# Optimization experiments

Hardware: AMD Instinct MI355X
Metric: run time of the kernel (lower is better)

The kernel has to match this reference:

```python
import jax, jax.numpy as jnp
import numpy as np

L = 8192            # sequence length
V = 100000          # vocab size
E = 256             # embedding dim
H = 512             # lstm hidden dim (bidirectional total)
HD = H // 2         # per-direction hidden
TAGS = 32
T = TAGS + 2        # tagset + START/STOP
START = T - 2       # START_TAG = -2
STOP = T - 1        # STOP_TAG = -1
NEG = -10000.0


def setup_inputs() -> dict:
    key = jax.random.key(0)
    ks = jax.random.split(key, 11)
    s = 0.05
    return {
        "input_words": jax.random.randint(ks[0], (L,), 0, V),
        "embed": jax.random.normal(ks[1], (V, E), dtype=jnp.float32) * s,
        "Wih_f": jax.random.normal(ks[2], (4 * HD, E), dtype=jnp.float32) * s,
        "Whh_f": jax.random.normal(ks[3], (4 * HD, HD), dtype=jnp.float32) * s,
        "b_f": jax.random.normal(ks[4], (4 * HD,), dtype=jnp.float32) * s,
        "Wih_b": jax.random.normal(ks[5], (4 * HD, E), dtype=jnp.float32) * s,
        "Whh_b": jax.random.normal(ks[6], (4 * HD, HD), dtype=jnp.float32) * s,
        "b_b": jax.random.normal(ks[7], (4 * HD,), dtype=jnp.float32) * s,
        "W_out": jax.random.normal(ks[8], (T, H), dtype=jnp.float32) * s,
        "b_out": jax.random.normal(ks[9], (T,), dtype=jnp.float32) * s,
        "transitions": jax.random.normal(ks[10], (T, T), dtype=jnp.float32),
    }


def _lstm_dir(x, Wih, Whh, b, reverse):
    # single-layer LSTM, one direction; torch gate order i, f, g, o
    def step(carry, xt):
        h, c = carry
        g = xt @ Wih.T + h @ Whh.T + b
        i, f, gg, o = jnp.split(g, 4)
        i = jax.nn.sigmoid(i)
        f = jax.nn.sigmoid(f)
        gg = jnp.tanh(gg)
        o = jax.nn.sigmoid(o)
        c = f * c + i * gg
        h = o * jnp.tanh(c)
        return (h, c), h

    init = (jnp.zeros((HD,), x.dtype), jnp.zeros((HD,), x.dtype))
    _, hs = jax.lax.scan(step, init, x, reverse=reverse)
    return hs  # (L, HD)


def _crf_marginals(feats, transitions):
    lse = jax.nn.logsumexp
    # forward algorithm: alpha_t[j] = lse_i(alpha_{t-1}[i] + trans[j,i]) + feat_t[j]
    def fstep(alpha, feat):
        new = lse(alpha[None, :] + transitions, axis=1) + feat
        return new, new

    alpha0 = jnp.full((T,), NEG, feats.dtype).at[START].set(0.0)
    alphaL, log_alpha = jax.lax.scan(fstep, alpha0, feats)  # (L, T)

    # backward algorithm, replicating repo's init: beta_L[j] = lse_i(trans[i, j])
    beta_last = lse(transitions, axis=0)

    # beta_t[j] = lse_i(beta_{t+1}[i] + feat_{t+1}[i] + trans[i, j])
    def bstep(beta, feat_next):
        new = lse((beta + feat_next)[:, None] + transitions, axis=0)
        return new, new

    _, betas = jax.lax.scan(bstep, beta_last, feats[1:], reverse=True)
    log_beta = jnp.concatenate([betas, beta_last[None]], axis=0)  # (L, T)
    return log_alpha + log_beta


def reference(input_words, embed, Wih_f, Whh_f, b_f, Wih_b, Whh_b, b_b,
              W_out, b_out, transitions):
    x = embed[input_words]                           # (L, E)
    hf = _lstm_dir(x, Wih_f, Whh_f, b_f, reverse=False)
    hb = _lstm_dir(x, Wih_b, Whh_b, b_b, reverse=True)
    lstm_out = jnp.concatenate([hf, hb], axis=-1)    # (L, H)
    feats = lstm_out @ W_out.T + b_out               # (L, T)
    score = _crf_marginals(feats, transitions)       # (L, T)
    tags = jnp.argmax(score, axis=1)                 # (L,)
    return score, tags
```

## Files before the change

kernel.cpp:

```cpp
#include <hip/hip_runtime.h>
#include <cstdint>
#include <cstddef>

#define LSEQ 8192
#define NT   34
#define NP   36
#define SCH  64
#define CCH  128
#define F_L2E 1.4426950408889634f
#define F_LN2 0.6931471805599453f

typedef int v4i __attribute__((ext_vector_type(4)));

#if __has_builtin(__builtin_amdgcn_global_load_lds)
#define HAS_GLL 1
#else
#define HAS_GLL 0
#endif

__device__ __forceinline__ float ex2(float x){
#if __has_builtin(__builtin_amdgcn_exp2f)
  return __builtin_amdgcn_exp2f(x);
#else
  return exp2f(x);
#endif
}
__device__ __forceinline__ float lg2(float x){
#if __has_builtin(__builtin_amdgcn_logf)
  return __builtin_amdgcn_logf(x);
#else
  return __log2f(x);
#endif
}

__device__ __forceinline__ float sigf(float x){
  return __fdividef(1.f, 1.f + ex2(-F_L2E * x));
}
__device__ __forceinline__ float tanhf_fast(float x){
  return 1.f - __fdividef(2.f, ex2(2.f * F_L2E * x) + 1.f);
}

__device__ __forceinline__ v4i mfma_i8(v4i a, v4i b, v4i c){
  asm("v_mfma_i32_16x16x64_i8 %0, %1, %2, %0" : "+v"(c) : "v"(a), "v"(b));
  return c;
}

__device__ __forceinline__ void barrier_lds(){
  asm volatile("s_waitcnt lgkmcnt(0)\n\ts_barrier" ::: "memory");
}

__global__ void k_quant(const float* __restrict__ Whh_f,
                        const float* __restrict__ Whh_b,
                        int* __restrict__ Wq, float* __restrict__ fac){
  int bid = blockIdx.x;
  int dir = bid >> 10;
  int r   = bid & 1023;
  int i   = threadIdx.x;
  const float* W = (dir ? Whh_b : Whh_f) + r * 256 + i * 4;
  float w0 = W[0], w1 = W[1], w2 = W[2], w3 = W[3];
  float m = fmaxf(fmaxf(fabsf(w0), fabsf(w1)), fmaxf(fabsf(w2), fabsf(w3)));
  for (int s = 32; s; s >>= 1) m = fmaxf(m, __shfl_xor(m, s));
  float scale = (m > 0.f) ? m / 127.f : 1.f;
  float inv = __fdividef(1.f, scale);
  int q0 = (int)rintf(w0 * inv), q1 = (int)rintf(w1 * inv);
  int q2 = (int)rintf(w2 * inv), q3 = (int)rintf(w3 * inv);
  q0 = max(-127, min(127, q0)); q1 = max(-127, min(127, q1));
  q2 = max(-127, min(127, q2)); q3 = max(-127, min(127, q3));
  int p = (q0 & 255) | ((q1 & 255) << 8) | ((q2 & 255) << 16) | ((q3 & 255) << 24);
  Wq[(dir << 16) + (r << 6) + i] = p;
  if (i == 0) fac[(dir << 10) + r] = scale * (1.f / 127.f);
}

__global__ void k_gproj(const int* __restrict__ words,
                        const float* __restrict__ embed,
                        const float* __restrict__ Wih_f, const float* __restrict__ b_f,
                        const float* __restrict__ Wih_b, const float* __restrict__ b_b,
                        float* __restrict__ G_f, float* __restrict__ G_b){
  int dir = blockIdx.y;
  const float* Wih = dir ? Wih_b : Wih_f;
  const float* bb  = dir ? b_b  : b_f;
  float* G = dir ? G_b : G_f;
  int t0 = blockIdx.x * 16;
  __shared__ __align__(16) float X[16 * 256];
  for (int idx = threadIdx.x; idx < 16 * 256; idx += 256) {
    int tt = idx >> 8, e = idx & 255;
    X[idx] = embed[(size_t)words[t0 + tt] * 256 + e];
  }
  __syncthreads();
  const float4* X4 = (const float4*)X;
  for (int rb = 0; rb < 4; rb++) {
    int r = rb * 256 + threadIdx.x;
    float bv = bb[r];
    float acc[16];
#pragma unroll
    for (int tt = 0; tt < 16; tt++) acc[tt] = bv;
    const float4* W4 = (const float4*)(Wih + (size_t)r * 256);
    for (int eb = 0; eb < 64; eb++) {
      float4 w = W4[eb];
#pragma unroll
      for (int tt = 0; tt < 16; tt++) {
        float4 x = X4[tt * 64 + eb];
        acc[tt] += w.x * x.x + w.y * x.y + w.z * x.z + w.w * x.w;
      }
    }
    for (int tt = 0; tt < 16; tt++)
      G[(size_t)(t0 + tt) * 1024 + (threadIdx.x << 2) + rb] = acc[tt];
  }
}

__global__ __launch_bounds__(512, 2) void k_lstm(const int* __restrict__ Wq,
                                                 const float* __restrict__ fac,
                                                 const float* __restrict__ G_f,
                                                 const float* __restrict__ G_b,
                                                 float* __restrict__ hf,
                                                 float* __restrict__ hb){
  int dir = blockIdx.x;
  const int* Wqd = Wq + (dir << 16);
  const float* facp = fac + (dir << 10);
  const float* G = dir ? G_b : G_f;
  float* hout = dir ? hb : hf;
  int tid = threadIdx.x;
  int ln  = tid & 63;
  int wv  = tid >> 6;
  int lg  = ln >> 4;
  int lr  = ln & 15;

  __shared__ __align__(16) float GL[2][4 * 1024];
  __shared__ __align__(16) int h8c[2][64];
  __shared__ __align__(16) int graw[1024];

  v4i wgt[4][2][4];
#pragma unroll
  for (int g = 0; g < 4; g++)
#pragma unroll
    for (int h = 0; h < 2; h++) {
      int R = g * 256 + wv * 32 + h * 16 + lr;
#pragma unroll
      for (int ks = 0; ks < 4; ks++)
        wgt[g][h][ks] = *(const v4i*)(Wqd + R * 64 + ks * 16 + lg * 4);
    }

  float fI = 0.f, fF = 0.f, fG = 0.f, fO = 0.f;
  if (tid < 256) {
    fI = facp[tid]; fF = facp[tid + 256];
    fG = facp[tid + 512]; fO = facp[tid + 768];
  }
  if (tid < 64) h8c[0][tid] = 0;
  float c = 0.f;
  v4i zero = {0, 0, 0, 0};

  auto stage = [&](int cn) {
    int half = cn & 1;
    int gt0 = dir ? (8191 - (cn * 4 + 3)) : (cn * 4);
    const char* src = (const char*)(G + (size_t)gt0 * 1024) + (wv << 11) + (ln << 4);
    char* dst = (char*)&GL[half][0] + (wv << 11);
#pragma unroll
    for (int i = 0; i < 2; i++) {
#if HAS_GLL
      __builtin_amdgcn_global_load_lds(
          (const __attribute__((address_space(1))) unsigned int*)(src + (i << 10)),
          (__attribute__((address_space(3))) unsigned int*)(dst + (i << 10)),
          16, 0, 0);
#else
      *(float4*)(dst + (i << 10) + (ln << 4)) = *(const float4*)(src + (i << 10));
#endif
    }
  };

  auto stepA = [&](const int* hbuf) {
    const v4i* hb4 = (const v4i*)hbuf;
    v4i b0 = hb4[lg], b1 = hb4[4 + lg], b2 = hb4[8 + lg], b3 = hb4[12 + lg];
#pragma unroll
    for (int g = 0; g < 4; g++)
#pragma unroll
      for (int h = 0; h < 2; h++) {
        v4i a = mfma_i8(wgt[g][h][0], b0, zero);
        a = mfma_i8(wgt[g][h][1], b1, a);
        a = mfma_i8(wgt[g][h][2], b2, a);
        a = mfma_i8(wgt[g][h][3], b3, a);
        if (lr == 0)
          *(v4i*)&graw[g * 256 + wv * 32 + h * 16 + lg * 4] = a;
      }
  };

  stage(0);
  asm volatile("s_waitcnt vmcnt(0)" ::: "memory");
  __syncthreads();

  int cur = 0;
  for (int cn = 0; cn < 2048; ++cn) {
    if (cn + 1 < 2048) stage(cn + 1);
    const float* Hc = GL[cn & 1];
#pragma unroll
    for (int s = 0; s < 4; ++s) {
      int row = dir ? (3 - s) : s;
      int t = (cn << 2) + s;
      stepA(h8c[cur]);
      barrier_lds();
      if (tid < 256) {
        int u = tid;
        int aI = graw[u], aF = graw[256 + u], aG = graw[512 + u], aO = graw[768 + u];
        float4 gv = ((const float4*)(Hc + (row << 10)))[u];
        float ri = (float)aI * fI + gv.x;
        float rf = (float)aF * fF + gv.y;
        float rg = (float)aG * fG + gv.z;
        float ro = (float)aO * fO + gv.w;
        float is = sigf(ri), fs = sigf(rf);
        float gt = tanhf_fast(rg), os = sigf(ro);
        c = fs * c + is * gt;
        float hv = os * tanhf_fast(c);
        int time = dir ? (8191 - t) : t;
        hout[(size_t)time * 256 + u] = hv;
        ((signed char*)h8c[cur ^ 1])[u] = (signed char)(int)rintf(hv * 127.f);
      }
      cur ^= 1;
      if (s == 3) {
        asm volatile("s_waitcnt vmcnt(0) lgkmcnt(0)\n\ts_barrier" ::: "memory");
      } else {
        barrier_lds();
      }
    }
  }
}

__global__ void k_feats(const float* __restrict__ hf, const float* __restrict__ hb,
                        const float* __restrict__ W_out, const float* __restrict__ b_out,
                        float* __restrict__ feats){
  int t0 = blockIdx.x * 16;
  for (int oi = threadIdx.x; oi < 16 * NT; oi += 256) {
    int tt = oi / NT;
    int tag = oi - tt * NT;
    int t = t0 + tt;
    const float4* w4 = (const float4*)(W_out + (size_t)tag * 512);
    const float4* a4 = (const float4*)(hf + (size_t)t * 256);
    const float4* c4 = (const float4*)(hb + (size_t)t * 256);
    float acc = b_out[tag];
    for (int k = 0; k < 64; k++) {
      float4 w = w4[k]; float4 h = a4[k];
      acc += w.x * h.x + w.y * h.y + w.z * h.z + w.w * h.w;
    }
    for (int k = 0; k < 64; k++) {
      float4 w = w4[64 + k]; float4 h = c4[k];
      acc += w.x * h.x + w.y * h.y + w.z * h.z + w.w * h.w;
    }
    feats[(size_t)t * NT + tag] = acc;
  }
}

__global__ __launch_bounds__(320) void k_crf_p1(const float* __restrict__ feats,
                                                const float* __restrict__ trans,
                                                float* __restrict__ Pg,
                                                float* __restrict__ rmaxG){
  int dir = blockIdx.x >> 7;
  int c   = blockIdx.x & (CCH - 1);
  int tid = threadIdx.x;
  int t0  = c * SCH;

  __shared__ __align__(16) float TRM[NT * NP];
  __shared__ float Fe[(SCH + 1) * NT];
  __shared__ __align__(16) float Pbuf[2][NT * NP];
  __shared__ float CM[NP];
  __shared__ float RMs[NT];

  for (int idx = tid; idx < NT * NT; idx += 320) {
    int j = idx / NT, k = idx - j * NT;
    float v = (dir == 0) ? trans[j * NT + k] : trans[k * NT + j];
    TRM[j * NP + k] = v * F_L2E;
  }
  for (int idx = tid; idx < (SCH + 1) * NT; idx += 320) {
    int s = idx / NT, j = idx - s * NT;
    int t = t0 + s; if (t > LSEQ - 1) t = LSEQ - 1;
    Fe[idx] = feats[(size_t)t * NT + j] * F_L2E;
  }
  for (int idx = tid; idx < NT * NP; idx += 320) {
    int k = idx / NP, i = idx - k * NP;
    Pbuf[0][idx] = (i < NT && i == k) ? 0.f : -1e30f;
  }
  if (tid < NP) CM[tid] = (tid < NT) ? 0.f : -1e30f;
  __syncthreads();
  if (tid < NT) {
    float m = -3e38f;
    for (int k = 0; k < NT; k++) m = fmaxf(m, TRM[tid * NP + k]);
    RMs[tid] = m;
  }
  __syncthreads();
  for (int idx = tid; idx < NT * NT; idx += 320) {
    int j = idx / NT, k = idx - j * NT;
    TRM[j * NP + k] -= RMs[j];
  }
  __syncthreads();

  int cur = 0;
  int j = tid / 9, g = tid - (tid / 9) * 9;
  bool act = (tid < 306);
  int i0 = 4 * g;

  for (int s = 0; s < SCH; s++) {
    int t = (dir == 0) ? (t0 + s) : (t0 + SCH - 1 - s);
    if (dir == 1 && t == LSEQ - 1) continue;
    const float* Pc = Pbuf[cur];
    float* Pn = Pbuf[cur ^ 1];
    if (act) {
      float cm0 = CM[i0], cm1 = CM[i0 + 1], cm2 = CM[i0 + 2], cm3 = CM[i0 + 3];
      float s0 = 0, s1 = 0, s2 = 0, s3 = 0;
      const float* trp = TRM + j * NP;
      const float* fep = Fe + (t + 1 - t0) * NT;
#pragma unroll
      for (int k = 0; k < NT; k++) {
        float trv = trp[k];
        if (dir == 1) trv += fep[k];
        float4 p = *(const float4*)&Pc[k * NP + i0];
        s0 += ex2(trv + p.x - cm0);
        s1 += ex2(trv + p.y - cm1);
        s2 += ex2(trv + p.z - cm2);
        s3 += ex2(trv + p.w - cm3);
      }
      float base = RMs[j] + ((dir == 0) ? Fe[(t - t0) * NT + j] : 0.f);
      float4 o;
      o.x = base + cm0 + lg2(s0);
      o.y = base + cm1 + lg2(s1);
      o.z = (i0 + 2 < NT) ? (base + cm2 + lg2(s2)) : -1e30f;
      o.w = (i0 + 3 < NT) ? (base + cm3 + lg2(s3)) : -1e30f;
      *(float4*)&Pn[j * NP + i0] = o;
    }
    __syncthreads();
    if (tid < NP) {
      float m = -3e38f;
      const float* col = Pn + tid;
      for (int k = 0; k < NT; k++) m = fmaxf(m, col[k * NP]);
      CM[tid] = m;
    }
    cur ^= 1;
    __syncthreads();
  }

  const float* Pf = Pbuf[cur];
  size_t base = (size_t)((dir << 7) + c) * (NT * NP);
  for (int idx = tid; idx < NT * NP; idx += 320)
    Pg[base + idx] = Pf[idx];
  if (tid < NT) {
    float m = -3e38f;
    for (int i = 0; i < NT; i++) m = fmaxf(m, Pf[tid * NP + i]);
    rmaxG[((dir << 7) + c) * NT + tid] = m;
  }
}

__global__ void k_crf_p2(const float* __restrict__ trans,
                         const float* __restrict__ Pg,
                         const float* __restrict__ rmaxG,
                         float* __restrict__ vIn){
  int dir = blockIdx.x;
  int lane = threadIdx.x;
  bool a = (lane < NT);
  int j = a ? lane : 0;
  __shared__ float V[NP];

  float v;
  if (dir == 0) {
    v = (lane == 32) ? 0.f : -10000.f * F_L2E;
  } else {
    float m = -3e38f;
    for (int i = 0; i < NT; i++) m = fmaxf(m, trans[i * NT + j]);
    float s = 0.f;
    for (int i = 0; i < NT; i++) s += ex2((trans[i * NT + j] - m) * F_L2E);
    v = m * F_L2E + lg2(s);
  }
  if (lane < NP) V[lane] = -1e30f;
  barrier_lds();
  if (a) V[j] = v;
  barrier_lds();
  float vm = a ? v : -3e38f;
  for (int off = 32; off; off >>= 1) vm = fmaxf(vm, __shfl_xor(vm, off));

  if (a) {
    int c0 = (dir == 0) ? 0 : (CCH - 1);
    vIn[((size_t)(dir << 7) + c0) * NP + j] = v;
  }

  for (int it = 0; it < CCH - 1; it++) {
    int c = (dir == 0) ? it : (CCH - 1 - it);
    const float* row = Pg + ((size_t)(dir << 7) + c) * (NT * NP) + j * NP;
    float rm = rmaxG[((dir << 7) + c) * NT + j];
    float m = rm + vm;
    float s = 0.f;
#pragma unroll
    for (int k = 0; k < NP; k += 4) {
      float4 p = *(const float4*)&row[k];
      s += ex2(p.x + V[k]     - m);
      s += ex2(p.y + V[k + 1] - m);
      s += ex2(p.z + V[k + 2] - m);
      s += ex2(p.w + V[k + 3] - m);
    }
    float nv = m + lg2(s);
    if (a) V[j] = nv;
    barrier_lds();
    float x = a ? nv : -3e38f;
    for (int off = 32; off; off >>= 1) x = fmaxf(x, __shfl_xor(x, off));
    vm = x;
    int cn = (dir == 0) ? (c + 1) : (c - 1);
    if (a) vIn[((size_t)(dir << 7) + cn) * NP + j] = nv;
  }
}

__global__ void k_crf_p3(const float* __restrict__ feats,
                         const float* __restrict__ trans,
                         const float* __restrict__ vIn,
                         float* __restrict__ wsA,
                         float* __restrict__ wsB){
  int dir = blockIdx.x >> 7;
  int c   = blockIdx.x & (CCH - 1);
  int lane = threadIdx.x;
  int t0 = c * SCH;
  bool a = (lane < NT);
  int j = a ? lane : 0;
  __shared__ float A[NP];
  __shared__ float U[NP];

  float trr[NT];
  float rm = -3e38f;
#pragma unroll
  for (int k = 0; k < NT; k++) {
    float vv = (dir == 0) ? trans[j * NT + k] : trans[k * NT + j];
    trr[k] = vv * F_L2E;
    rm = fmaxf(rm, trr[k]);
  }
  if (lane < NP) { A[lane] = -1e30f; U[lane] = -1e30f; }
  float v0 = vIn[((size_t)(dir << 7) + c) * NP + j];
  barrier_lds();
  if (a) A[j] = v0;
  barrier_lds();
  float am = a ? v0 : -3e38f;
  for (int off = 32; off; off >>= 1) am = fmaxf(am, __shfl_xor(am, off));

  if (dir == 0) {
    float fe = feats[(size_t)t0 * NT + j] * F_L2E;
    for (int s = 0; s < SCH; s++) {
      int t = t0 + s;
      int tn = (t + 1 < LSEQ) ? t + 1 : LSEQ - 1;
      float fe_n = feats[(size_t)tn * NT + j] * F_L2E;
      float m = rm + am;
      float ss = 0.f;
#pragma unroll
      for (int k = 0; k < NT; k++) ss += ex2(trr[k] + A[k] - m);
      float out = m + lg2(ss) + fe;
      if (a) wsA[(size_t)t * NT + j] = out * F_LN2;
      if (a) A[j] = out;
      barrier_lds();
      float x = a ? out : -3e38f;
      for (int off = 32; off; off >>= 1) x = fmaxf(x, __shfl_xor(x, off));
      am = x;
      fe = fe_n;
    }
  } else {
    float b = v0;
    int tfirst = t0 + SCH; if (tfirst > LSEQ - 1) tfirst = LSEQ - 1;
    float fe = feats[(size_t)tfirst * NT + j] * F_L2E;
    for (int s = 0; s < SCH; s++) {
      int t = t0 + SCH - 1 - s;
      float fe_n = feats[(size_t)t * NT + j] * F_L2E;
      float out;
      if (t == LSEQ - 1) {
        out = b;
      } else {
        if (a) U[j] = b + fe;
        barrier_lds();
        float um = a ? U[j] : -3e38f;
        for (int off = 32; off; off >>= 1) um = fmaxf(um, __shfl_xor(um, off));
        float m = rm + um;
        float ss = 0.f;
#pragma unroll
        for (int k = 0; k < NT; k++) ss += ex2(trr[k] + U[k] - m);
        out = m + lg2(ss);
        barrier_lds();
      }
      if (a) wsB[(size_t)t * NT + j] = out * F_LN2;
      b = out;
      fe = fe_n;
    }
  }
}

__global__ void k_finish(const float* __restrict__ wsA, const float* __restrict__ wsB,
                         float* __restrict__ out){
  int t = blockIdx.x * 256 + threadIdx.x;
  float m = -3e38f; int bi = 0;
  for (int i = 0; i < NT; i++) {
    float sc = wsA[(size_t)t * NT + i] + wsB[(size_t)t * NT + i];
    out[(size_t)t * NT + i] = sc;
    if (sc > m) { m = sc; bi = i; }
  }
  out[(size_t)LSEQ * NT + t] = (float)bi;
}

extern "C" void kernel_launch(void* const* d_in, const int* in_sizes, int n_in,
                              void* d_out, int out_size, void* d_ws, size_t ws_size,
                              hipStream_t stream) {
  const int*   words  = (const int*)  d_in[0];
  const float* embed  = (const float*)d_in[1];
  const float* Wih_f  = (const float*)d_in[2];
  const float* Whh_f  = (const float*)d_in[3];
  const float* b_f    = (const float*)d_in[4];
  const float* Wih_b  = (const float*)d_in[5];
  const float* Whh_b  = (const float*)d_in[6];
  const float* b_b    = (const float*)d_in[7];
  const float* W_out  = (const float*)d_in[8];
  const float* b_out  = (const float*)d_in[9];
  const float* trans  = (const float*)d_in[10];
  float* out = (float*)d_out;

  float* wsf = (float*)d_ws;
  size_t off = 0;
  float* G_f   = wsf + off; off += (size_t)LSEQ * 1024;
  float* G_b   = wsf + off; off += (size_t)LSEQ * 1024;
  float* hf    = wsf + off; off += (size_t)LSEQ * 256;
  float* hb    = wsf + off; off += (size_t)LSEQ * 256;
  float* feats = wsf + off; off += (size_t)LSEQ * NT + 16;
  float* wsA   = wsf + off; off += (size_t)LSEQ * NT + 16;
  float* wsB   = wsf + off; off += (size_t)LSEQ * NT + 16;
  float* fac   = wsf + off; off += 2048;
  int*   Wq    = (int*)(wsf + off); off += 2 * 1024 * 64;
  float* Pg    = G_f;
  float* rmaxG = G_f + 256 * (NT * NP);
  float* vIn   = rmaxG + 256 * NT + 32;

  k_quant<<<2048, 64, 0, stream>>>(Whh_f, Whh_b, Wq, fac);
  k_gproj<<<dim3(512, 2), 256, 0, stream>>>(words, embed, Wih_f, b_f, Wih_b, b_b, G_f, G_b);
  k_lstm<<<2, 512, 0, stream>>>(Wq, fac, G_f, G_b, hf, hb);
  k_feats<<<512, 256, 0, stream>>>(hf, hb, W_out, b_out, feats);
  k_crf_p1<<<256, 320, 0, stream>>>(feats, trans, Pg, rmaxG);
  k_crf_p2<<<2, 64, 0, stream>>>(trans, Pg, rmaxG, vIn);
  k_crf_p3<<<256, 64, 0, stream>>>(feats, trans, vIn, wsA, wsB);
  k_finish<<<32, 256, 0, stream>>>(wsA, wsB, out);
}
```

Measured before the change: 8.705 ms.

## Apply LSTM gate nonlinearities in MFMA registers, removing LDS gate round-trip and barrier

Each lane now takes its gate pre-activations straight from the MFMA result registers by selecting the right row and component, instead of writing them to a shared graw buffer, synchronising, and reading them back. All 512 threads compute the cell update redundantly (two lanes per unit) and pack the int8 hidden state with DPP lane adds before one lane writes it. This removes one LDS barrier and the graw traffic from each recurrent step on the serial critical path. The cost is redundant transcendental work and extra register pressure at two blocks per CU. It also moves to the compiler MFMA builtin so the compiler can schedule around the hazards itself.

```diff
diff --git a/kernel.cpp b/kernel.cpp
--- a/kernel.cpp
+++ b/kernel.cpp
@@ -18,6 +18,17 @@
 #define HAS_GLL 0
 #endif
 
+#if __has_builtin(__builtin_amdgcn_mfma_i32_16x16x64_i8)
+#define MFMA_I8(a,b,c) __builtin_amdgcn_mfma_i32_16x16x64_i8((a),(b),(c),0,0,0)
+#else
+__device__ __forceinline__ v4i mfma_i8_asm(v4i a, v4i b, v4i c){
+  asm volatile("v_mfma_i32_16x16x64_i8 %0, %1, %2, %0\n\ts_nop 7\n\ts_nop 7"
+               : "+v"(c) : "v"(a), "v"(b));
+  return c;
+}
+#define MFMA_I8(a,b,c) mfma_i8_asm((a),(b),(c))
+#endif
+
 __device__ __forceinline__ float ex2(float x){
 #if __has_builtin(__builtin_amdgcn_exp2f)
   return __builtin_amdgcn_exp2f(x);
@@ -38,11 +49,6 @@
 }
 __device__ __forceinline__ float tanhf_fast(float x){
   return 1.f - __fdividef(2.f, ex2(2.f * F_L2E * x) + 1.f);
-}
-
-__device__ __forceinline__ v4i mfma_i8(v4i a, v4i b, v4i c){
-  asm("v_mfma_i32_16x16x64_i8 %0, %1, %2, %0" : "+v"(c) : "v"(a), "v"(b));
-  return c;
 }
 
 __device__ __forceinline__ void barrier_lds(){
@@ -124,27 +130,25 @@
   int wv  = tid >> 6;
   int lg  = ln >> 4;
   int lr  = ln & 15;
+  int h_l = (lr >> 2) & 1;
+  int r_l = lr & 3;
+  int u   = (wv << 5) + (h_l << 4) + (lg << 2) + r_l;
 
   __shared__ __align__(16) float GL[2][4 * 1024];
   __shared__ __align__(16) int h8c[2][64];
-  __shared__ __align__(16) int graw[1024];
 
   v4i wgt[4][2][4];
 #pragma unroll
   for (int g = 0; g < 4; g++)
 #pragma unroll
     for (int h = 0; h < 2; h++) {
-      int R = g * 256 + wv * 32 + h * 16 + lr;
+      int R = g * 256 + (wv << 5) + (h << 4) + lr;
 #pragma unroll
       for (int ks = 0; ks < 4; ks++)
         wgt[g][h][ks] = *(const v4i*)(Wqd + R * 64 + ks * 16 + lg * 4);
     }
 
-  float fI = 0.f, fF = 0.f, fG = 0.f, fO = 0.f;
-  if (tid < 256) {
-    fI = facp[tid]; fF = facp[tid + 256];
-    fG = facp[tid + 512]; fO = facp[tid + 768];
-  }
+  float fI = facp[u], fF = facp[u + 256], fG = facp[u + 512], fO = facp[u + 768];
   if (tid < 64) h8c[0][tid] = 0;
   float c = 0.f;
   v4i zero = {0, 0, 0, 0};
@@ -167,20 +171,54 @@
     }
   };
 
-  auto stepA = [&](const int* hbuf) {
-    const v4i* hb4 = (const v4i*)hbuf;
+  auto step = [&](int t, const float* Grow, const int* bufR, int* bufW) {
+    const v4i* hb4 = (const v4i*)bufR;
     v4i b0 = hb4[lg], b1 = hb4[4 + lg], b2 = hb4[8 + lg], b3 = hb4[12 + lg];
+    float4 gv = ((const float4*)Grow)[u];
+    v4i res[4][2];
 #pragma unroll
     for (int g = 0; g < 4; g++)
 #pragma unroll
       for (int h = 0; h < 2; h++) {
-        v4i a = mfma_i8(wgt[g][h][0], b0, zero);
-        a = mfma_i8(wgt[g][h][1], b1, a);
-        a = mfma_i8(wgt[g][h][2], b2, a);
-        a = mfma_i8(wgt[g][h][3], b3, a);
-        if (lr == 0)
-          *(v4i*)&graw[g * 256 + wv * 32 + h * 16 + lg * 4] = a;
+        v4i a = MFMA_I8(wgt[g][h][0], b0, zero);
+        a = MFMA_I8(wgt[g][h][1], b1, a);
+        a = MFMA_I8(wgt[g][h][2], b2, a);
+        a = MFMA_I8(wgt[g][h][3], b3, a);
+        res[g][h] = a;
       }
+    bool sh = h_l != 0;
+    bool s1 = (r_l & 1) != 0;
+    bool s2 = (r_l & 2) != 0;
+    v4i tI = sh ? res[0][1] : res[0][0];
+    v4i tF = sh ? res[1][1] : res[1][0];
+    v4i tG = sh ? res[2][1] : res[2][0];
+    v4i tO = sh ? res[3][1] : res[3][0];
+    int vI = s2 ? (s1 ? tI.w : tI.z) : (s1 ? tI.y : tI.x);
+    int vF = s2 ? (s1 ? tF.w : tF.z) : (s1 ? tF.y : tF.x);
+    int vG = s2 ? (s1 ? tG.w : tG.z) : (s1 ? tG.y : tG.x);
+    int vO = s2 ? (s1 ? tO.w : tO.z) : (s1 ? tO.y : tO.x);
+    float ri = (float)vI * fI + gv.x;
+    float rf = (float)vF * fF + gv.y;
+    float rg = (float)vG * fG + gv.z;
+    float ro = (float)vO * fO + gv.w;
+    float is = sigf(ri), fs = sigf(rf);
+    float gt = tanhf_fast(rg), os = sigf(ro);
+    c = fs * c + is * gt;
+    float hv = os * tanhf_fast(c);
+    if (lr < 8) {
+      int time = dir ? (8191 - t) : t;
+      hout[(size_t)time * 256 + u] = hv;
+    }
+    int q = ((int)rintf(hv * 127.f)) & 255;
+    int x = q << (r_l * 8);
+#if __has_builtin(__builtin_amdgcn_mov_dpp)
+    x += __builtin_amdgcn_mov_dpp(x, 0xB1, 0xF, 0xF, true);
+    x += __builtin_amdgcn_mov_dpp(x, 0x4E, 0xF, 0xF, true);
+#else
+    x += __shfl_xor(x, 1);
+    x += __shfl_xor(x, 2);
+#endif
+    if (r_l == 0 && lr < 8) bufW[u >> 2] = x;
   };
 
   stage(0);
@@ -194,25 +232,7 @@
 #pragma unroll
     for (int s = 0; s < 4; ++s) {
       int row = dir ? (3 - s) : s;
-      int t = (cn << 2) + s;
-      stepA(h8c[cur]);
-      barrier_lds();
-      if (tid < 256) {
-        int u = tid;
-        int aI = graw[u], aF = graw[256 + u], aG = graw[512 + u], aO = graw[768 + u];
-        float4 gv = ((const float4*)(Hc + (row << 10)))[u];
-        float ri = (float)aI * fI + gv.x;
-        float rf = (float)aF * fF + gv.y;
-        float rg = (float)aG * fG + gv.z;
-        float ro = (float)aO * fO + gv.w;
-        float is = sigf(ri), fs = sigf(rf);
-        float gt = tanhf_fast(rg), os = sigf(ro);
-        c = fs * c + is * gt;
-        float hv = os * tanhf_fast(c);
-        int time = dir ? (8191 - t) : t;
-        hout[(size_t)time * 256 + u] = hv;
-        ((signed char*)h8c[cur ^ 1])[u] = (signed char)(int)rintf(hv * 127.f);
-      }
+      step((cn << 2) + s, Hc + (row << 10), h8c[cur], h8c[cur ^ 1]);
       cur ^= 1;
       if (s == 3) {
         asm volatile("s_waitcnt vmcnt(0) lgkmcnt(0)\n\ts_barrier" ::: "memory");
```

Measured after the change: 8.389 ms. 3.6% less time.
